# Optimization experiments

Hardware: AMD Instinct MI355X
Metric: run time of the kernel (lower is better)

The kernel has to match this reference:

```python
import jax, jax.numpy as jnp
import numpy as np

DIM = 1024
HEADS = 16
EPS = 1e-05
B, T, C, H, W = 2, 16, DIM, 32, 32


def setup_inputs() -> dict:
    key = jax.random.key(0)
    ks = jax.random.split(key, 4)
    s = 1.0 / np.sqrt(DIM)
    return {
        "x": jax.random.normal(ks[0], (B, T, C, H, W), dtype=jnp.float32),
        "ln_w": jnp.ones((C,), dtype=jnp.float32),
        "ln_b": jnp.zeros((C,), dtype=jnp.float32),
        "Wq": jax.random.normal(ks[1], (C, C), dtype=jnp.float32) * s,
        "Wk": jax.random.normal(ks[2], (C, C), dtype=jnp.float32) * s,
        "Wv": jax.random.normal(ks[3], (C, C), dtype=jnp.float32) * s,
    }


def reference(x, ln_w, ln_b, Wq, Wk, Wv):
    b, t, c, h, w = x.shape
    heads = HEADS
    dh = c // heads
    scale = dh ** (-0.5)

    # Channel LayerNorm: normalize over C per (b,t,h,w)
    xc = jnp.transpose(x, (0, 1, 3, 4, 2))  # [B,T,H,W,C]
    mu = jnp.mean(xc, axis=-1, keepdims=True)
    var = jnp.mean(jnp.square(xc - mu), axis=-1, keepdims=True)
    xn = (xc - mu) * jax.lax.rsqrt(var + EPS) * ln_w + ln_b  # [B,T,H,W,C]

    # Q/K from spatial mean-pool
    pooled = jnp.mean(xn, axis=(2, 3))  # [B,T,C]
    q = pooled @ Wq.T  # [B,T,C]
    k = pooled @ Wk.T  # [B,T,C]

    # V per pixel; torch permutes to [B,W,H,T,C] then flattens W-major
    v = jnp.transpose(xn, (0, 3, 2, 1, 4)).reshape(b, h * w, t, c)  # [B,HW(w-major),T,C]
    v = v @ Wv.T

    q = q.reshape(b, t, heads, dh).transpose(0, 2, 1, 3) * scale  # [B,h,T,dh]
    k = k.reshape(b, t, heads, dh).transpose(0, 2, 3, 1)          # [B,h,dh,T]
    v = v.reshape(b, h * w, t, heads, dh).transpose(0, 1, 3, 2, 4)  # [B,HW,h,T,dh]

    attn = jax.nn.softmax(jnp.matmul(q, k), axis=-1)  # [B,h,T,T]
    out = jnp.einsum('bhst,bnhtd->bnhsd', attn, v)    # [B,HW,h,T,dh]
    # permute(0,3,2,4,1) -> [B,T,h,dh,HW], then view as (H,W)
    out = out.transpose(0, 3, 2, 4, 1).reshape(b, t, c, h, w)
    return out
```

## Files before the change

kernel.cpp:

```cpp
#include <hip/hip_runtime.h>
#include <stdint.h>
#include <stddef.h>

#define CDIM 1024
#define HWD  1024
#define TD   16
#define BD   2
#define NH   16
#define DHD  64

typedef __attribute__((ext_vector_type(8))) short bf16x8;
typedef __attribute__((ext_vector_type(4))) short bf16x4;
typedef __attribute__((ext_vector_type(4))) float f32x4;

static __device__ __forceinline__ short f2bf(float f) {
  uint32_t u = __builtin_bit_cast(uint32_t, f);
  uint32_t r = (u + 0x7FFFu + ((u >> 16) & 1u)) >> 16;
  return (short)(uint16_t)r;
}
static __device__ __forceinline__ float bf2f(short s) {
  return __builtin_bit_cast(float, (uint32_t)((uint16_t)s) << 16);
}

static __device__ __forceinline__ void gl_lds16(const short* g, short* l) {
  __builtin_amdgcn_global_load_lds((const __attribute__((address_space(1))) unsigned int*)g,
                                   (__attribute__((address_space(3))) unsigned int*)l,
                                   16, 0, 0);
}

__global__ void k_cast3(const float* __restrict__ Wq, const float* __restrict__ Wk,
                        const float* __restrict__ Wv, short* __restrict__ Wqkb,
                        short* __restrict__ Wb) {
  int bid = blockIdx.x;
  int mat = bid >> 10;
  const float* src = mat == 0 ? Wq : (mat == 1 ? Wk : Wv);
  short* dst = mat == 0 ? Wqkb : (mat == 1 ? Wqkb + 1048576 : Wb);
  int i = ((bid & 1023) * 256 + threadIdx.x) * 4;
  f32x4 v = *(const f32x4*)&src[i];
  dst[i + 0] = f2bf(v[0]);
  dst[i + 1] = f2bf(v[1]);
  dst[i + 2] = f2bf(v[2]);
  dst[i + 3] = f2bf(v[3]);
}

__global__ __launch_bounds__(512) void k_ln(const float* __restrict__ x,
                                            const float* __restrict__ lnw,
                                            const float* __restrict__ lnb,
                                            short* __restrict__ xnT,
                                            float* __restrict__ part) {
  int bt = blockIdx.y;
  int pg = blockIdx.x;
  int P0 = pg * 64;
  int tid = threadIdx.x;
  int pq = tid & 15, cr = tid >> 4;
  int pbase = P0 + pq * 4;
  const float* xs = x + (size_t)bt * CDIM * HWD;
  short* outB = xnT + (size_t)bt * CDIM * HWD;

  __shared__ __align__(16) char lbuf[2 * 32 * 65 * 4];
  float* redA = (float*)lbuf;
  float* redB = redA + 32 * 65;
  short* tile = (short*)lbuf;
  __shared__ float muS[64], rsS[64];

  float s[4] = {}, s2[4] = {};
  #pragma unroll
  for (int j = 0; j < 32; ++j) {
    int c = cr + 32 * j;
    f32x4 v = *(const f32x4*)&xs[(size_t)c * HWD + pbase];
    #pragma unroll
    for (int i = 0; i < 4; ++i) { s[i] += v[i]; s2[i] += v[i] * v[i]; }
  }
  #pragma unroll
  for (int i = 0; i < 4; ++i) {
    redA[cr * 65 + pq * 4 + i] = s[i];
    redB[cr * 65 + pq * 4 + i] = s2[i];
  }
  __syncthreads();
  if (tid < 64) {
    float a = 0.f, b2 = 0.f;
    #pragma unroll
    for (int k = 0; k < 32; ++k) { a += redA[k * 65 + tid]; b2 += redB[k * 65 + tid]; }
    float mu = a * (1.0f / CDIM);
    float var = b2 * (1.0f / CDIM) - mu * mu;
    muS[tid] = mu;
    rsS[tid] = rsqrtf(var + 1e-5f);
  }
  __syncthreads();
  float mu_[4], rs_[4];
  #pragma unroll
  for (int i = 0; i < 4; ++i) { mu_[i] = muS[pq * 4 + i]; rs_[i] = rsS[pq * 4 + i]; }

  for (int h = 0; h < 8; ++h) {
    #pragma unroll
    for (int jj = 0; jj < 4; ++jj) {
      int cl = cr + 32 * jj;
      int c = h * 128 + cl;
      f32x4 v = *(const f32x4*)&xs[(size_t)c * HWD + pbase];
      float w = lnw[c], bb = lnb[c];
      int cc = cl >> 3, c7 = cl & 7;
      float psum = 0.f;
      #pragma unroll
      for (int i = 0; i < 4; ++i) {
        int px = pq * 4 + i;
        float xn = (v[i] - mu_[i]) * rs_[i] * w + bb;
        psum += xn;
        tile[px * 130 + ((cc ^ (px & 7)) << 3) + c7] = f2bf(xn);
      }
      psum += __shfl_xor(psum, 1, 64);
      psum += __shfl_xor(psum, 2, 64);
      psum += __shfl_xor(psum, 4, 64);
      psum += __shfl_xor(psum, 8, 64);
      if (pq == 0)
        part[((size_t)(bt * 16 + pg)) * CDIM + c] = psum;
    }
    __syncthreads();
    {
      int qr = tid & 63, sg = tid >> 6;
      int q = (qr & 31) * 32 + pg * 2 + (qr >> 5);
      short* dst = outB + (size_t)q * CDIM + h * 128 + sg * 16;
      #pragma unroll
      for (int mm = 0; mm < 2; ++mm) {
        int cc = sg * 2 + mm;
        bf16x8 vv = *(const bf16x8*)&tile[qr * 130 + ((cc ^ (qr & 7)) << 3)];
        *(bf16x8*)&dst[mm * 8] = vv;
      }
    }
    __syncthreads();
  }
}

__global__ void k_pool_red(const float* __restrict__ part, short* __restrict__ pooledb) {
  int bt = blockIdx.y;
  int c = blockIdx.x * 256 + threadIdx.x;
  float s = 0.f;
  #pragma unroll
  for (int pc = 0; pc < 16; ++pc) s += part[((size_t)(bt * 16 + pc)) * CDIM + c];
  pooledb[bt * CDIM + c] = f2bf(s * (1.0f / HWD));
}

__global__ __launch_bounds__(256) void k_qk_mfma(const short* __restrict__ Wqkb,
                                                 const short* __restrict__ pooledb,
                                                 float* __restrict__ qm,
                                                 float* __restrict__ km) {
  int n0 = blockIdx.x * 128;
  __shared__ __align__(16) short lA[32 * 32];
  __shared__ __align__(16) short lB[128 * 32];
  int tid = threadIdx.x, lane = tid & 63, wid = tid >> 6;
  int s0 = wid * 128 + lane, s1 = s0 + 64;
  int fr = lane & 15, fk = (lane >> 4) * 8;
  f32x4 acc[2][2] = {};

  for (int kt = 0; kt < CDIM / 32; ++kt) {
    int k0 = kt * 32;
    __syncthreads();
    gl_lds16(&Wqkb[(size_t)(n0 + (s0 >> 2)) * CDIM + k0 + (s0 & 3) * 8], &lB[s0 * 8]);
    gl_lds16(&Wqkb[(size_t)(n0 + (s1 >> 2)) * CDIM + k0 + (s1 & 3) * 8], &lB[s1 * 8]);
    if (wid < 2) {
      gl_lds16(&pooledb[(size_t)(tid >> 2) * CDIM + k0 + (tid & 3) * 8], &lA[tid * 8]);
    }
    __syncthreads();
    bf16x8 af[2], bfr[2];
    #pragma unroll
    for (int mi = 0; mi < 2; ++mi)
      af[mi] = *(const bf16x8*)&lA[(mi * 16 + fr) * 32 + fk];
    #pragma unroll
    for (int ni = 0; ni < 2; ++ni)
      bfr[ni] = *(const bf16x8*)&lB[(wid * 32 + ni * 16 + fr) * 32 + fk];
    #pragma unroll
    for (int mi = 0; mi < 2; ++mi)
      #pragma unroll
      for (int ni = 0; ni < 2; ++ni)
        acc[mi][ni] = __builtin_amdgcn_mfma_f32_16x16x32_bf16(af[mi], bfr[ni], acc[mi][ni], 0, 0, 0);
  }

  int cr = lane >> 4;
  #pragma unroll
  for (int mi = 0; mi < 2; ++mi)
    #pragma unroll
    for (int ni = 0; ni < 2; ++ni)
      #pragma unroll
      for (int rr = 0; rr < 4; ++rr) {
        int row = mi * 16 + cr * 4 + rr;
        int col = n0 + wid * 32 + ni * 16 + fr;
        float v = acc[mi][ni][rr];
        if (col < 1024) qm[(size_t)row * CDIM + col] = v;
        else            km[(size_t)row * CDIM + col - 1024] = v;
      }
}

__global__ void k_attn(const float* __restrict__ qm, const float* __restrict__ km,
                       float* __restrict__ attn) {
  int bg = blockIdx.x;
  int b = bg >> 4, g = bg & 15;
  int s = threadIdx.x >> 4, t = threadIdx.x & 15;
  const float* qr = qm + (size_t)(b * TD + s) * CDIM + g * DHD;
  const float* kr = km + (size_t)(b * TD + t) * CDIM + g * DHD;
  float d = 0.f;
  #pragma unroll
  for (int i = 0; i < DHD; ++i) d += qr[i] * kr[i];
  d *= 0.125f;
  float m = d;
  #pragma unroll
  for (int off = 8; off; off >>= 1) m = fmaxf(m, __shfl_xor(m, off, 16));
  float e = __expf(d - m);
  float sum = e;
  #pragma unroll
  for (int off = 8; off; off >>= 1) sum += __shfl_xor(sum, off, 16);
  attn[(size_t)bg * 256 + s * 16 + t] = e / sum;
}

__global__ __launch_bounds__(512, 2) void k_vgemm(const short* __restrict__ Wb,
                                                  const short* __restrict__ xnT,
                                                  short* __restrict__ vp) {
  int bid = blockIdx.x;
  int swz = (bid & 7) * 64 + (bid >> 3);
  int bt = swz >> 4;
  int m0 = ((swz >> 2) & 3) * 256;
  int n0 = (swz & 3) * 256;
  const short* Bm = xnT + (size_t)bt * CDIM * HWD;

  __shared__ __align__(16) short lA[2][256 * 64];
  __shared__ __align__(16) short lB[2][256 * 64];

  int tid = threadIdx.x, lane = tid & 63, wid = tid >> 6;
  int wm = wid >> 2, wn = wid & 3;

  int srow = wid * 8 + (lane >> 3);
  int schunk = (lane & 7) ^ (lane >> 3);
  const short* gA = Wb + (size_t)(m0 + srow) * CDIM + schunk * 8;
  const short* gB = Bm + (size_t)(n0 + srow) * CDIM + schunk * 8;
  int doff = wid * 512 + lane * 8;

  int fr = lane & 15, klane = lane >> 4;
  int c0 = ((klane ^ (fr & 7)) * 8);
  int rA = (wm * 128 + fr) * 64;
  int rB = (wn * 64 + fr) * 64;

  f32x4 acc[8][4] = {};
  bf16x8 bq[4], af[4];

#define ISSUE(p, kt1, nb)                                                      \
  do {                                                                         \
    gl_lds16(gA + (size_t)(p) * 64 * CDIM + (kt1) * 64, &lA[nb][(p) * 4096 + doff]); \
    gl_lds16(gB + (size_t)(p) * 64 * CDIM + (kt1) * 64, &lB[nb][(p) * 4096 + doff]); \
  } while (0)
#define RDA(mi, ks, b) (*(const bf16x8*)&lA[b][rA + (mi) * 1024 + (c0 ^ ((ks) * 32))])
#define RDB(ni, ks, b) (*(const bf16x8*)&lB[b][rB + (ni) * 1024 + (c0 ^ ((ks) * 32))])

  ISSUE(0, 0, 0); ISSUE(1, 0, 0); ISSUE(2, 0, 0); ISSUE(3, 0, 0);

  for (int kt = 0; kt < 16; ++kt) {
    int cur = kt & 1, nxt = cur ^ 1;
    bool st = (kt + 1 < 16);
    if (st) {
      ISSUE(0, kt + 1, nxt);
      asm volatile("s_waitcnt vmcnt(2)" ::: "memory");
    } else {
      asm volatile("s_waitcnt vmcnt(0)" ::: "memory");
    }
    __builtin_amdgcn_s_barrier();
    #pragma unroll
    for (int ni = 0; ni < 4; ++ni) bq[ni] = RDB(ni, 0, cur);
    #pragma unroll
    for (int mi = 0; mi < 4; ++mi) af[mi] = RDA(mi, 0, cur);
    __builtin_amdgcn_s_setprio(1);
    #pragma unroll
    for (int mi = 0; mi < 4; ++mi)
      #pragma unroll
      for (int ni = 0; ni < 4; ++ni)
        acc[mi][ni] = __builtin_amdgcn_mfma_f32_16x16x32_bf16(af[mi], bq[ni], acc[mi][ni], 0, 0, 0);
    __builtin_amdgcn_s_setprio(0);
    __builtin_amdgcn_s_barrier();
    #pragma unroll
    for (int mi = 0; mi < 4; ++mi) af[mi] = RDA(4 + mi, 0, cur);
    if (st) ISSUE(1, kt + 1, nxt);
    __builtin_amdgcn_s_barrier();
    __builtin_amdgcn_s_setprio(1);
    #pragma unroll
    for (int mi = 0; mi < 4; ++mi)
      #pragma unroll
      for (int ni = 0; ni < 4; ++ni)
        acc[4 + mi][ni] = __builtin_amdgcn_mfma_f32_16x16x32_bf16(af[mi], bq[ni], acc[4 + mi][ni], 0, 0, 0);
    __builtin_amdgcn_s_setprio(0);
    __builtin_amdgcn_s_barrier();
    #pragma unroll
    for (int ni = 0; ni < 4; ++ni) bq[ni] = RDB(ni, 1, cur);
    #pragma unroll
    for (int mi = 0; mi < 4; ++mi) af[mi] = RDA(mi, 1, cur);
    if (st) ISSUE(2, kt + 1, nxt);
    __builtin_amdgcn_s_barrier();
    __builtin_amdgcn_s_setprio(1);
    #pragma unroll
    for (int mi = 0; mi < 4; ++mi)
      #pragma unroll
      for (int ni = 0; ni < 4; ++ni)
        acc[mi][ni] = __builtin_amdgcn_mfma_f32_16x16x32_bf16(af[mi], bq[ni], acc[mi][ni], 0, 0, 0);
    __builtin_amdgcn_s_setprio(0);
    __builtin_amdgcn_s_barrier();
    #pragma unroll
    for (int mi = 0; mi < 4; ++mi) af[mi] = RDA(4 + mi, 1, cur);
    if (st) ISSUE(3, kt + 1, nxt);
    __builtin_amdgcn_s_barrier();
    __builtin_amdgcn_s_setprio(1);
    #pragma unroll
    for (int mi = 0; mi < 4; ++mi)
      #pragma unroll
      for (int ni = 0; ni < 4; ++ni)
        acc[4 + mi][ni] = __builtin_amdgcn_mfma_f32_16x16x32_bf16(af[mi], bq[ni], acc[4 + mi][ni], 0, 0, 0);
    __builtin_amdgcn_s_setprio(0);
    __builtin_amdgcn_s_barrier();
  }
#undef ISSUE
#undef RDA
#undef RDB

  short* outB = vp + (size_t)bt * CDIM * HWD;
  int cr = lane >> 4;
  #pragma unroll
  for (int mi = 0; mi < 8; ++mi)
    #pragma unroll
    for (int ni = 0; ni < 4; ++ni)
      #pragma unroll
      for (int r = 0; r < 4; ++r) {
        int row = m0 + wm * 128 + mi * 16 + cr * 4 + r;
        int col = n0 + wn * 64 + ni * 16 + fr;
        outB[(size_t)row * HWD + col] = f2bf(acc[mi][ni][r]);
      }
}

__global__ __launch_bounds__(256) void k_mix(const short* __restrict__ vp,
                                             const float* __restrict__ attn,
                                             float* __restrict__ out) {
  int c = blockIdx.x;
  int b = blockIdx.y;
  int g = c >> 6;
  __shared__ __align__(16) short vpl[TD * HWD];
  __shared__ float at[256];
  int tid = threadIdx.x;
  at[tid] = attn[(size_t)(b * NH + g) * 256 + tid];
  #pragma unroll
  for (int j = 0; j < 8; ++j) {
    int chunk = j * 256 + tid;
    int t = chunk >> 7, qc = chunk & 127;
    bf16x8 v = *(const bf16x8*)&vp[((size_t)(b * TD + t) * CDIM + c) * HWD + qc * 8];
    *(bf16x8*)&vpl[t * HWD + qc * 8] = v;
  }
  __syncthreads();
  int p = tid * 4;
  #pragma unroll
  for (int sh = 0; sh < 2; ++sh) {
    f32x4 acc[8] = {};
    #pragma unroll
    for (int t = 0; t < TD; ++t) {
      bf16x4 v4 = *(const bf16x4*)&vpl[t * HWD + p];
      f32x4 vf = {bf2f(v4[0]), bf2f(v4[1]), bf2f(v4[2]), bf2f(v4[3])};
      #pragma unroll
      for (int s8 = 0; s8 < 8; ++s8) {
        float a = at[(sh * 8 + s8) * 16 + t];
        acc[s8] += a * vf;
      }
    }
    #pragma unroll
    for (int s8 = 0; s8 < 8; ++s8) {
      int s = sh * 8 + s8;
      *(f32x4*)&out[((size_t)(b * TD + s) * CDIM + c) * HWD + p] = acc[s8];
    }
  }
}

extern "C" void kernel_launch(void* const* d_in, const int* in_sizes, int n_in,
                              void* d_out, int out_size, void* d_ws, size_t ws_size,
                              hipStream_t stream) {
  const float* x   = (const float*)d_in[0];
  const float* lnw = (const float*)d_in[1];
  const float* lnb = (const float*)d_in[2];
  const float* Wq  = (const float*)d_in[3];
  const float* Wk  = (const float*)d_in[4];
  const float* Wv  = (const float*)d_in[5];
  float* out = (float*)d_out;

  char* ws = (char*)d_ws;
  const size_t XNT_OFF   = 0;
  const size_t VP_OFF    = XNT_OFF + 67108864;
  const size_t WB_OFF    = VP_OFF + 67108864;
  const size_t WQKB_OFF  = WB_OFF + 2097152;
  const size_t POOLB_OFF = WQKB_OFF + 4194304;
  const size_t QM_OFF    = POOLB_OFF + 65536;
  const size_t KM_OFF    = QM_OFF + 131072;
  const size_t ATTN_OFF  = KM_OFF + 131072;

  short* xnT    = (short*)(ws + XNT_OFF);
  short* vp     = (short*)(ws + VP_OFF);
  float* part   = (float*)(ws + VP_OFF);
  short* Wb     = (short*)(ws + WB_OFF);
  short* Wqkb   = (short*)(ws + WQKB_OFF);
  short* poolb  = (short*)(ws + POOLB_OFF);
  float* qm     = (float*)(ws + QM_OFF);
  float* km     = (float*)(ws + KM_OFF);
  float* attn   = (float*)(ws + ATTN_OFF);

  k_cast3<<<dim3(3072), 256, 0, stream>>>(Wq, Wk, Wv, Wqkb, Wb);
  k_ln<<<dim3(16, 32), 512, 0, stream>>>(x, lnw, lnb, xnT, part);
  k_pool_red<<<dim3(4, 32), 256, 0, stream>>>(part, poolb);
  k_qk_mfma<<<dim3(16), 256, 0, stream>>>(Wqkb, poolb, qm, km);
  k_attn<<<dim3(32), 256, 0, stream>>>(qm, km, attn);
  k_vgemm<<<dim3(512), 512, 0, stream>>>(Wb, xnT, vp);
  k_mix<<<dim3(1024, 2), 256, 0, stream>>>(vp, attn, out);
}
```

Baseline: 222.2 us.

## Replace pipelined 256x256 V-GEMM with simple single-buffered 128x128 tile kernel

Rewrites the V projection GEMM to use 128x128 output tiles with 256 threads and K-steps of 32, loading into a single LDS buffer between two barriers. It drops the double-buffered prefetch, the interleaved issue/compute schedule, the wave priority hints and the block swizzle. Smaller tiles raise the block count and occupancy but give less data reuse. The copy-compute overlap is also gone, so memory latency is exposed on every K step.

```diff
diff --git a/kernel.cpp b/kernel.cpp
--- a/kernel.cpp
+++ b/kernel.cpp
@@ -210,121 +210,63 @@
   attn[(size_t)bg * 256 + s * 16 + t] = e / sum;
 }
 
-__global__ __launch_bounds__(512, 2) void k_vgemm(const short* __restrict__ Wb,
-                                                  const short* __restrict__ xnT,
-                                                  short* __restrict__ vp) {
-  int bid = blockIdx.x;
-  int swz = (bid & 7) * 64 + (bid >> 3);
-  int bt = swz >> 4;
-  int m0 = ((swz >> 2) & 3) * 256;
-  int n0 = (swz & 3) * 256;
+__global__ __launch_bounds__(256) void k_vgemm(const short* __restrict__ Wb,
+                                               const short* __restrict__ xnT,
+                                               short* __restrict__ vp) {
+  int bt = blockIdx.z;
+  int m0 = blockIdx.y * 128;
+  int n0 = blockIdx.x * 128;
+  const short* A = Wb;
   const short* Bm = xnT + (size_t)bt * CDIM * HWD;
-
-  __shared__ __align__(16) short lA[2][256 * 64];
-  __shared__ __align__(16) short lB[2][256 * 64];
-
-  int tid = threadIdx.x, lane = tid & 63, wid = tid >> 6;
-  int wm = wid >> 2, wn = wid & 3;
-
-  int srow = wid * 8 + (lane >> 3);
-  int schunk = (lane & 7) ^ (lane >> 3);
-  const short* gA = Wb + (size_t)(m0 + srow) * CDIM + schunk * 8;
-  const short* gB = Bm + (size_t)(n0 + srow) * CDIM + schunk * 8;
-  int doff = wid * 512 + lane * 8;
-
-  int fr = lane & 15, klane = lane >> 4;
-  int c0 = ((klane ^ (fr & 7)) * 8);
-  int rA = (wm * 128 + fr) * 64;
-  int rB = (wn * 64 + fr) * 64;
-
-  f32x4 acc[8][4] = {};
-  bf16x8 bq[4], af[4];
-
-#define ISSUE(p, kt1, nb)                                                      \
-  do {                                                                         \
-    gl_lds16(gA + (size_t)(p) * 64 * CDIM + (kt1) * 64, &lA[nb][(p) * 4096 + doff]); \
-    gl_lds16(gB + (size_t)(p) * 64 * CDIM + (kt1) * 64, &lB[nb][(p) * 4096 + doff]); \
-  } while (0)
-#define RDA(mi, ks, b) (*(const bf16x8*)&lA[b][rA + (mi) * 1024 + (c0 ^ ((ks) * 32))])
-#define RDB(ni, ks, b) (*(const bf16x8*)&lB[b][rB + (ni) * 1024 + (c0 ^ ((ks) * 32))])
-
-  ISSUE(0, 0, 0); ISSUE(1, 0, 0); ISSUE(2, 0, 0); ISSUE(3, 0, 0);
-
-  for (int kt = 0; kt < 16; ++kt) {
-    int cur = kt & 1, nxt = cur ^ 1;
-    bool st = (kt + 1 < 16);
-    if (st) {
-      ISSUE(0, kt + 1, nxt);
-      asm volatile("s_waitcnt vmcnt(2)" ::: "memory");
-    } else {
-      asm volatile("s_waitcnt vmcnt(0)" ::: "memory");
-    }
-    __builtin_amdgcn_s_barrier();
-    #pragma unroll
-    for (int ni = 0; ni < 4; ++ni) bq[ni] = RDB(ni, 0, cur);
-    #pragma unroll
-    for (int mi = 0; mi < 4; ++mi) af[mi] = RDA(mi, 0, cur);
-    __builtin_amdgcn_s_setprio(1);
+  __shared__ __align__(16) short lA[128 * 32];
+  __shared__ __align__(16) short lB[128 * 32];
+  int tid = threadIdx.x;
+  int lane = tid & 63;
+  int wid = tid >> 6;
+  int wr = (wid >> 1) * 64;
+  int wc = (wid & 1) * 64;
+  f32x4 acc[4][4] = {};
+
+  int sm = tid >> 2;
+  int slc = ((tid & 3) ^ ((tid >> 3) & 3)) * 8;
+  const short* gA = A + (size_t)(m0 + sm) * CDIM + slc;
+  const short* gB = Bm + (size_t)(n0 + sm) * CDIM + slc;
+  short* dA = &lA[tid * 8];
+  short* dB = &lB[tid * 8];
+  int fr = lane & 15;
+  int c0 = (((lane >> 4) ^ ((fr >> 1) & 3)) * 8);
+
+  for (int kt = 0; kt < CDIM / 32; ++kt) {
+    __syncthreads();
+    gl_lds16(gA + kt * 32, dA);
+    gl_lds16(gA + kt * 32 + (size_t)64 * CDIM, dA + 64 * 32);
+    gl_lds16(gB + kt * 32, dB);
+    gl_lds16(gB + kt * 32 + (size_t)64 * CDIM, dB + 64 * 32);
+    __syncthreads();
+    bf16x8 af[4], bfr[4];
     #pragma unroll
     for (int mi = 0; mi < 4; ++mi)
+      af[mi] = *(const bf16x8*)&lA[(wr + mi * 16 + fr) * 32 + c0];
+    #pragma unroll
+    for (int ni = 0; ni < 4; ++ni)
+      bfr[ni] = *(const bf16x8*)&lB[(wc + ni * 16 + fr) * 32 + c0];
+    #pragma unroll
+    for (int mi = 0; mi < 4; ++mi)
       #pragma unroll
       for (int ni = 0; ni < 4; ++ni)
-        acc[mi][ni] = __builtin_amdgcn_mfma_f32_16x16x32_bf16(af[mi], bq[ni], acc[mi][ni], 0, 0, 0);
-    __builtin_amdgcn_s_setprio(0);
-    __builtin_amdgcn_s_barrier();
-    #pragma unroll
-    for (int mi = 0; mi < 4; ++mi) af[mi] = RDA(4 + mi, 0, cur);
-    if (st) ISSUE(1, kt + 1, nxt);
-    __builtin_amdgcn_s_barrier();
-    __builtin_amdgcn_s_setprio(1);
-    #pragma unroll
-    for (int mi = 0; mi < 4; ++mi)
-      #pragma unroll
-      for (int ni = 0; ni < 4; ++ni)
-        acc[4 + mi][ni] = __builtin_amdgcn_mfma_f32_16x16x32_bf16(af[mi], bq[ni], acc[4 + mi][ni], 0, 0, 0);
-    __builtin_amdgcn_s_setprio(0);
-    __builtin_amdgcn_s_barrier();
-    #pragma unroll
-    for (int ni = 0; ni < 4; ++ni) bq[ni] = RDB(ni, 1, cur);
-    #pragma unroll
-    for (int mi = 0; mi < 4; ++mi) af[mi] = RDA(mi, 1, cur);
-    if (st) ISSUE(2, kt + 1, nxt);
-    __builtin_amdgcn_s_barrier();
-    __builtin_amdgcn_s_setprio(1);
-    #pragma unroll
-    for (int mi = 0; mi < 4; ++mi)
-      #pragma unroll
-      for (int ni = 0; ni < 4; ++ni)
-        acc[mi][ni] = __builtin_amdgcn_mfma_f32_16x16x32_bf16(af[mi], bq[ni], acc[mi][ni], 0, 0, 0);
-    __builtin_amdgcn_s_setprio(0);
-    __builtin_amdgcn_s_barrier();
-    #pragma unroll
-    for (int mi = 0; mi < 4; ++mi) af[mi] = RDA(4 + mi, 1, cur);
-    if (st) ISSUE(3, kt + 1, nxt);
-    __builtin_amdgcn_s_barrier();
-    __builtin_amdgcn_s_setprio(1);
-    #pragma unroll
-    for (int mi = 0; mi < 4; ++mi)
-      #pragma unroll
-      for (int ni = 0; ni < 4; ++ni)
-        acc[4 + mi][ni] = __builtin_amdgcn_mfma_f32_16x16x32_bf16(af[mi], bq[ni], acc[4 + mi][ni], 0, 0, 0);
-    __builtin_amdgcn_s_setprio(0);
-    __builtin_amdgcn_s_barrier();
-  }
-#undef ISSUE
-#undef RDA
-#undef RDB
+        acc[mi][ni] = __builtin_amdgcn_mfma_f32_16x16x32_bf16(af[mi], bfr[ni], acc[mi][ni], 0, 0, 0);
+  }
 
   short* outB = vp + (size_t)bt * CDIM * HWD;
   int cr = lane >> 4;
   #pragma unroll
-  for (int mi = 0; mi < 8; ++mi)
+  for (int mi = 0; mi < 4; ++mi)
     #pragma unroll
     for (int ni = 0; ni < 4; ++ni)
       #pragma unroll
       for (int r = 0; r < 4; ++r) {
-        int row = m0 + wm * 128 + mi * 16 + cr * 4 + r;
-        int col = n0 + wn * 64 + ni * 16 + fr;
+        int row = m0 + wr + mi * 16 + cr * 4 + r;
+        int col = n0 + wc + ni * 16 + fr;
         outB[(size_t)row * HWD + col] = f2bf(acc[mi][ni][r]);
       }
 }
@@ -405,6 +347,6 @@
   k_pool_red<<<dim3(4, 32), 256, 0, stream>>>(part, poolb);
   k_qk_mfma<<<dim3(16), 256, 0, stream>>>(Wqkb, poolb, qm, km);
   k_attn<<<dim3(32), 256, 0, stream>>>(qm, km, attn);
-  k_vgemm<<<dim3(512), 512, 0, stream>>>(Wb, xnT, vp);
+  k_vgemm<<<dim3(8, 8, 32), 256, 0, stream>>>(Wb, xnT, vp);
   k_mix<<<dim3(1024, 2), 256, 0, stream>>>(vp, attn, out);
 }
```

After: 211.4 us, median of 2. -4.8%, faster.
